# Kernel tuning notes

Hardware: AMD Instinct MI355X
Metric: run time of the kernel (lower is better)

Reference implementation:

```python
import math
import jax, jax.numpy as jnp
import numpy as np

B, V, D, H, DE, DFF = 2, 2048, 1024, 16, 256, 4096
DK = D // H


def setup_inputs() -> dict:
    key = jax.random.key(0)
    ks = jax.random.split(key, 24)
    n = lambda k, shape, s=0.02: (jax.random.normal(k, shape, jnp.float32) * s)
    z = lambda *shape: jnp.zeros(shape, jnp.float32)
    return {
        'x': jax.random.normal(ks[0], (B, V, D), jnp.float32),
        'e_node': jax.random.normal(ks[1], (B, V, DE), jnp.float32),
        'conn': jax.random.uniform(ks[2], (B, V, V), jnp.float32),
        'ln1_g': jnp.ones((D,), jnp.float32), 'ln1_b': z(D),
        'f1w1': n(ks[3], (DE, 2 * D)), 'f1b1': z(2 * D),
        'f1w2': n(ks[4], (2 * D, 2 * D)), 'f1b2': z(2 * D),
        'wq': n(ks[5], (D, D)), 'bq': z(D),
        'wk': n(ks[6], (D, D)), 'bk': z(D),
        'wv': n(ks[7], (D, D)), 'bv': z(D),
        'wp': n(ks[8], (D, D)), 'bp': z(D),
        'ln2_g': jnp.ones((D,), jnp.float32), 'ln2_b': z(D),
        'f2w1': n(ks[9], (DE, 2 * D)), 'f2b1': z(2 * D),
        'f2w2': n(ks[10], (2 * D, 2 * D)), 'f2b2': z(2 * D),
        'ffw1': n(ks[11], (D, DFF)), 'ffb1': z(DFF),
        'ffw2': n(ks[12], (DFF, D)), 'ffb2': z(D),
    }


def _ln(x, g, b):
    m = x.mean(-1, keepdims=True)
    v = ((x - m) ** 2).mean(-1, keepdims=True)
    return (x - m) / jnp.sqrt(v + 1e-5) * g + b


def _film(e, w1, b1, w2, b2):
    h = jax.nn.gelu(e @ w1 + b1, approximate=False)  # torch F.gelu default = exact erf
    gb = h @ w2 + b2
    return jnp.split(gb, 2, axis=-1)  # gamma, beta


def reference(x, e_node, conn, ln1_g, ln1_b, f1w1, f1b1, f1w2, f1b2,
              wq, bq, wk, bk, wv, bv, wp, bp, ln2_g, ln2_b,
              f2w1, f2b1, f2w2, f2b2, ffw1, ffb1, ffw2, ffb2):
    b, v, d = x.shape
    # Pre-norm + FiLM 1
    y = _ln(x, ln1_g, ln1_b)
    g1, be1 = _film(e_node, f1w1, f1b1, f1w2, f1b2)
    y = y * (1.0 + g1) + be1
    # Multi-head attention with additive log(conn) mask
    heads = lambda t: t.reshape(b, v, H, DK).transpose(0, 2, 1, 3)  # [B,h,V,dk]
    Q = heads(y @ wq + bq)
    K = heads(y @ wk + bk)
    Vv = heads(y @ wv + bv)
    logits = jnp.einsum('bhqd,bhkd->bhqk', Q, K) / math.sqrt(DK)
    log_mask = jnp.log(jnp.clip(conn, 0.0, 1.0) + 1e-6)[:, None]  # [B,1,V,V]
    s = logits + log_mask
    s = s - s.max(-1, keepdims=True)
    a = jnp.exp(s)
    a = a / (a.sum(-1, keepdims=True) + 1e-8)
    o = jnp.einsum('bhqk,bhkd->bhqd', a, Vv)
    o = o.transpose(0, 2, 1, 3).reshape(b, v, d)
    x = x + (o @ wp + bp)
    # Pre-norm + FiLM 2 + FFN
    y2 = _ln(x, ln2_g, ln2_b)
    g2, be2 = _film(e_node, f2w1, f2b1, f2w2, f2b2)
    y2 = y2 * (1.0 + g2) + be2
    y2 = jax.nn.gelu(y2 @ ffw1 + ffb1, approximate=False) @ ffw2 + ffb2
    return x + y2
```

## Files before the change

kernel.cpp:

```cpp
#include <hip/hip_runtime.h>
#include <math.h>
#include <stdint.h>

#define B_   2
#define V_   2048
#define D_   1024
#define H_   16
#define DK_  64
#define DE_  256
#define DFF_ 4096
#define M_   (B_*V_)
#define D2_  (2*D_)
#define D3_  (3*D_)

typedef unsigned short u16;
typedef unsigned int   u32;
typedef __bf16 bf16x8 __attribute__((ext_vector_type(8)));
typedef u16    u16x8  __attribute__((ext_vector_type(8)));
typedef u16    u16x4  __attribute__((ext_vector_type(4)));
typedef float  f32x4  __attribute__((ext_vector_type(4)));
typedef u32    u32x2  __attribute__((ext_vector_type(2)));
typedef u32    u32x4  __attribute__((ext_vector_type(4)));

__device__ __forceinline__ float bf2f(u16 u) {
    union { unsigned int i; float f; } z; z.i = ((unsigned int)u) << 16; return z.f;
}
__device__ __forceinline__ u16 f2bf(float f) {
    union { float f; unsigned int i; } z; z.f = f;
    unsigned int x = z.i;
    return (u16)((x + 0x7fffu + ((x >> 16) & 1u)) >> 16);
}
__device__ __forceinline__ float gelu_erf(float v) {
    return 0.5f * v * (1.0f + erff(v * 0.70710678118654752f));
}
__device__ __forceinline__ float ldv(const float* p) { return *p; }
__device__ __forceinline__ float ldv(const u16* p)   { return bf2f(*p); }
__device__ __forceinline__ void  stv(float* p, float v) { *p = v; }
__device__ __forceinline__ void  stv(u16* p,   float v) { *p = f2bf(v); }

__device__ __forceinline__ void gload16(const u16* g, u16* lds)
{
    __builtin_amdgcn_global_load_lds(
        (const __attribute__((address_space(1))) void*)g,
        (__attribute__((address_space(3))) void*)(uintptr_t)lds,
        16, 0, 0);
}

__device__ __forceinline__ void barrier_raw()
{
    asm volatile("" ::: "memory");
    __builtin_amdgcn_s_barrier();
    asm volatile("" ::: "memory");
}

__global__ void convT_k(const float* __restrict__ W, u16* __restrict__ Wt, int K, int N)
{
    __shared__ float tile[32][33];
    const int n0 = blockIdx.x * 32, k0 = blockIdx.y * 32;
    const int tx = threadIdx.x, ty = threadIdx.y;
    #pragma unroll
    for (int j = 0; j < 4; ++j)
        tile[ty * 4 + j][tx] = W[(size_t)(k0 + ty * 4 + j) * N + n0 + tx];
    __syncthreads();
    #pragma unroll
    for (int j = 0; j < 4; ++j)
        Wt[(size_t)(n0 + ty * 4 + j) * K + k0 + tx] = f2bf(tile[tx][ty * 4 + j]);
}

__global__ void conv_k(const float* __restrict__ X, u16* __restrict__ Y)
{
    const int i = (blockIdx.x * 256 + threadIdx.x) * 4;
    f32x4 v = *reinterpret_cast<const f32x4*>(X + i);
    u16x4 o;
    #pragma unroll
    for (int j = 0; j < 4; ++j) o[j] = f2bf(v[j]);
    *reinterpret_cast<u16x4*>(Y + i) = o;
}

__global__ void lmask_k(const float* __restrict__ conn, u16* __restrict__ Lm)
{
    const size_t i = ((size_t)blockIdx.x * 256 + threadIdx.x) * 8;
    f32x4 a = *reinterpret_cast<const f32x4*>(conn + i);
    f32x4 b = *reinterpret_cast<const f32x4*>(conn + i + 4);
    u16x8 o;
    #pragma unroll
    for (int j = 0; j < 4; ++j) {
        o[j]     = f2bf(__log2f(fminf(fmaxf(a[j], 0.f), 1.f) + 1e-6f));
        o[j + 4] = f2bf(__log2f(fminf(fmaxf(b[j], 0.f), 1.f) + 1e-6f));
    }
    *reinterpret_cast<u16x8*>(Lm + i) = o;
}

__global__ void qkvbias_k(const float* __restrict__ bq, const float* __restrict__ bk,
                          const float* __restrict__ bv, float* __restrict__ o)
{
    int i = blockIdx.x * 256 + threadIdx.x;
    o[i] = i < 1024 ? bq[i] : (i < 2048 ? bk[i - 1024] : bv[i - 2048]);
}

template<int EPI, int BN, typename TC, typename TRES>
__launch_bounds__(256)
__global__ void gemm_k(const u16* __restrict__ A, const u16* __restrict__ Wt,
                       const float* __restrict__ bias, const TRES* __restrict__ res,
                       TC* __restrict__ C, int M, int N, int K)
{
    constexpr int NB = BN / 32;
    constexpr int IB = BN / 32;
    __shared__ u16 As[2][128 * 64];
    __shared__ u16 Bs[2][BN * 64];

    const int tid  = threadIdx.x;
    const int lane = tid & 63;
    const int w    = tid >> 6;
    const int wm   = (w >> 1) * 64, wn = (w & 1) * (BN / 2);
    const int m0   = blockIdx.y * 128, n0 = blockIdx.x * BN;
    const int l15  = lane & 15, l4 = lane >> 4;
    const int rStage = lane >> 3;

    int rrA[4], ccA[4];
    #pragma unroll
    for (int i = 0; i < 4; ++i) {
        rrA[i] = w * 32 + i * 8 + rStage;
        ccA[i] = (lane & 7) ^ (rrA[i] & 7);
    }
    int rrB[IB], ccB[IB];
    #pragma unroll
    for (int i = 0; i < IB; ++i) {
        rrB[i] = w * (BN / 4) + i * 8 + rStage;
        ccB[i] = (lane & 7) ^ (rrB[i] & 7);
    }

    auto stage = [&](int kt, int dd) {
        const int k0 = kt * 64;
        #pragma unroll
        for (int i = 0; i < 4; ++i)
            gload16(A + (size_t)(m0 + rrA[i]) * K + k0 + ccA[i] * 8, &As[dd][w * 2048 + i * 512]);
        #pragma unroll
        for (int i = 0; i < IB; ++i)
            gload16(Wt + (size_t)(n0 + rrB[i]) * K + k0 + ccB[i] * 8, &Bs[dd][w * (BN * 16) + i * 512]);
    };

    f32x4 acc[4][NB] = {};
    const int NT = K / 64;

    stage(0, 0);

    for (int t = 0; t < NT; ++t) {
        const int d = t & 1;
        barrier_raw();
        if (t + 1 < NT) {
            stage(t + 1, d ^ 1);
            if constexpr (BN == 128) asm volatile("s_waitcnt vmcnt(8)" ::: "memory");
            else                     asm volatile("s_waitcnt vmcnt(6)" ::: "memory");
        } else {
            asm volatile("s_waitcnt vmcnt(0)" ::: "memory");
        }
        barrier_raw();
        __builtin_amdgcn_sched_barrier(0);

        #pragma unroll
        for (int kk = 0; kk < 2; ++kk) {
            bf16x8 a[4], b[NB];
            #pragma unroll
            for (int mb = 0; mb < 4; ++mb) {
                int r  = wm + mb * 16 + l15;
                int ph = (kk * 4 + l4) ^ (r & 7);
                a[mb] = *reinterpret_cast<const bf16x8*>(&As[d][r * 64 + ph * 8]);
            }
            #pragma unroll
            for (int nb = 0; nb < NB; ++nb) {
                int r  = wn + nb * 16 + l15;
                int ph = (kk * 4 + l4) ^ (r & 7);
                b[nb] = *reinterpret_cast<const bf16x8*>(&Bs[d][r * 64 + ph * 8]);
            }
            #pragma unroll
            for (int mb = 0; mb < 4; ++mb)
                #pragma unroll
                for (int nb = 0; nb < NB; ++nb)
                    acc[mb][nb] = __builtin_amdgcn_mfma_f32_16x16x32_bf16(a[mb], b[nb], acc[mb][nb], 0, 0, 0);
        }
    }

    #pragma unroll
    for (int nb = 0; nb < NB; ++nb) {
        int col = n0 + wn + nb * 16 + l15;
        float bv = bias[col];
        #pragma unroll
        for (int mb = 0; mb < 4; ++mb) {
            #pragma unroll
            for (int i = 0; i < 4; ++i) {
                int row = m0 + wm + mb * 16 + l4 * 4 + i;
                float v = acc[mb][nb][i] + bv;
                if (EPI == 1) v = gelu_erf(v);
                if (EPI == 2) v += ldv(res + (size_t)row * N + col);
                stv(C + (size_t)row * N + col, v);
            }
        }
    }
}

template<typename TX>
__launch_bounds__(256)
__global__ void lnfilm_k(const TX* __restrict__ X, const u16* __restrict__ GB,
                         const float* __restrict__ g, const float* __restrict__ bb,
                         u16* __restrict__ Y)
{
    const int row = blockIdx.x;
    const int tid = threadIdx.x;
    const int d0  = tid * 4;
    const TX* xr = X + (size_t)row * D_ + d0;
    float xs[4], s = 0.f, sq = 0.f;
    if constexpr (sizeof(TX) == 4) {
        f32x4 v4 = *reinterpret_cast<const f32x4*>(xr);
        #pragma unroll
        for (int j = 0; j < 4; ++j) { xs[j] = v4[j]; s += xs[j]; sq += xs[j] * xs[j]; }
    } else {
        u16x4 v4 = *reinterpret_cast<const u16x4*>(xr);
        #pragma unroll
        for (int j = 0; j < 4; ++j) { xs[j] = bf2f(v4[j]); s += xs[j]; sq += xs[j] * xs[j]; }
    }
    #pragma unroll
    for (int off = 32; off; off >>= 1) {
        s  += __shfl_xor(s, off);
        sq += __shfl_xor(sq, off);
    }
    __shared__ float rs[4], rq[4];
    const int w = tid >> 6;
    if ((tid & 63) == 0) { rs[w] = s; rq[w] = sq; }
    __syncthreads();
    s  = rs[0] + rs[1] + rs[2] + rs[3];
    sq = rq[0] + rq[1] + rq[2] + rq[3];
    const float mean = s * (1.0f / D_);
    const float var  = sq * (1.0f / D_) - mean * mean;
    const float rstd = rsqrtf(fmaxf(var, 0.f) + 1e-5f);
    const u16* gbr = GB + (size_t)row * D2_ + d0;
    u16x4 g4 = *reinterpret_cast<const u16x4*>(gbr);
    u16x4 b4 = *reinterpret_cast<const u16x4*>(gbr + D_);
    f32x4 gg = *reinterpret_cast<const f32x4*>(g + d0);
    f32x4 bv = *reinterpret_cast<const f32x4*>(bb + d0);
    u16x4 o;
    #pragma unroll
    for (int j = 0; j < 4; ++j) {
        float v = (xs[j] - mean) * rstd * gg[j] + bv[j];
        v = v * (1.0f + bf2f(g4[j])) + bf2f(b4[j]);
        o[j] = f2bf(v);
    }
    *reinterpret_cast<u16x4*>(Y + (size_t)row * D_ + d0) = o;
}

__launch_bounds__(256)
__global__ void attn_k(const u16* __restrict__ Q, const u16* __restrict__ K,
                       const u16* __restrict__ Vv, const u16* __restrict__ Lm,
                       u16* __restrict__ O, int ld)
{
    __shared__ u16 Ks[64 * 64];
    __shared__ u16 Vs[64 * 64];
    __shared__ u16 Lms[128 * 64];
    __shared__ u16 Ps[128 * 72];

    const int blk = blockIdx.x;
    const int qt  = blk & 15;
    const int h   = (blk >> 4) & 15;
    const int b   = blk >> 8;
    const int q0  = qt * 128;
    const int tid = threadIdx.x, lane = tid & 63, w = tid >> 6;
    const int l15 = lane & 15, l4 = lane >> 4;
    const size_t bV = (size_t)b * V_;

    bf16x8 qa[2][2];
    #pragma unroll
    for (int g = 0; g < 2; ++g) {
        const u16* qp = Q + (bV + q0 + w * 32 + g * 16 + l15) * ld + h * 64;
        u16x8 r0 = *reinterpret_cast<const u16x8*>(qp + l4 * 8);
        u16x8 r1 = *reinterpret_cast<const u16x8*>(qp + 32 + l4 * 8);
        u16x8 s0, s1;
        #pragma unroll
        for (int j = 0; j < 8; ++j) {
            s0[j] = f2bf(bf2f(r0[j]) * 0.125f);
            s1[j] = f2bf(bf2f(r1[j]) * 0.125f);
        }
        union { u16x8 u; bf16x8 h; } c0, c1;
        c0.u = s0; c1.u = s1;
        qa[g][0] = c0.h; qa[g][1] = c1.h;
    }

    const int rStage = (lane >> 3);
    const int cSw    = ((lane & 7) ^ rStage) * 8;
    const int vK     = ((lane >> 5) << 2) + ((lane & 7) >> 1);
    const int vDk    = ((lane >> 3) & 3) * 16 + (lane & 1) * 8;
    const u32 vaddr  = (u32)(uintptr_t)&Vs[0] + (l4 << 10) + (l15 << 3);

    int lmOff[4];
    #pragma unroll
    for (int kb = 0; kb < 4; ++kb)
        lmOff[kb] = ((((kb << 1) | (l4 >> 1)) ^ (l15 & 7)) << 3);

    const float LOG2E = 1.44269504088896f;
    float lrp[2] = {0.f, 0.f};
    f32x4 o4[2][4] = {};

    for (int kt = 0; kt < V_ / 64; ++kt) {
        const int k0 = kt * 64;
        if (kt) __syncthreads();
        #pragma unroll
        for (int i = 0; i < 2; ++i) {
            int r  = i * 32 + w * 8 + rStage;
            int kv = i * 32 + w * 8 + vK;
            gload16(K  + (bV + k0 + r)  * ld + h * 64 + cSw, &Ks[i * 2048 + w * 512]);
            gload16(Vv + (bV + k0 + kv) * ld + h * 64 + vDk, &Vs[i * 2048 + w * 512]);
        }
        #pragma unroll
        for (int i = 0; i < 4; ++i) {
            int r = i * 32 + w * 8 + rStage;
            gload16(Lm + (bV + q0 + r) * (size_t)V_ + k0 + cSw, &Lms[i * 2048 + w * 512]);
        }
        __syncthreads();

        #pragma unroll
        for (int g = 0; g < 2; ++g) {
            f32x4 s[4];
            #pragma unroll
            for (int kb = 0; kb < 4; ++kb) {
                int row = (kb * 16 + l15) * 64;
                bf16x8 k0f = *reinterpret_cast<const bf16x8*>(&Ks[row + ((l4 ^ (l15 & 7)) * 8)]);
                bf16x8 k1f = *reinterpret_cast<const bf16x8*>(&Ks[row + (((l4 + 4) ^ (l15 & 7)) * 8)]);
                f32x4 z = {};
                z = __builtin_amdgcn_mfma_f32_16x16x32_bf16(k0f, qa[g][0], z, 0, 0, 0);
                z = __builtin_amdgcn_mfma_f32_16x16x32_bf16(k1f, qa[g][1], z, 0, 0, 0);
                s[kb] = z;
            }
            const int lmRow = w * 32 + g * 16 + l15;
            const u16* lmBase = &Lms[lmRow * 64 + (l4 & 1) * 4];
            u16* psW = &Ps[lmRow * 72 + l4 * 4];
            #pragma unroll
            for (int kb = 0; kb < 4; ++kb) {
                u16x4 lm4 = *reinterpret_cast<const u16x4*>(lmBase + lmOff[kb]);
                float p0, p1, p2, p3;
                float t0 = fmaf(s[kb][0], LOG2E, bf2f(lm4[0]));
                float t1 = fmaf(s[kb][1], LOG2E, bf2f(lm4[1]));
                float t2 = fmaf(s[kb][2], LOG2E, bf2f(lm4[2]));
                float t3 = fmaf(s[kb][3], LOG2E, bf2f(lm4[3]));
                asm("v_exp_f32 %0, %1" : "=v"(p0) : "v"(t0));
                asm("v_exp_f32 %0, %1" : "=v"(p1) : "v"(t1));
                asm("v_exp_f32 %0, %1" : "=v"(p2) : "v"(t2));
                asm("v_exp_f32 %0, %1" : "=v"(p3) : "v"(t3));
                lrp[g] += (p0 + p1) + (p2 + p3);
                u32 d0, d1;
                asm("v_cvt_pk_bf16_f32 %0, %1, %2" : "=v"(d0) : "v"(p0), "v"(p1));
                asm("v_cvt_pk_bf16_f32 %0, %1, %2" : "=v"(d1) : "v"(p2), "v"(p3));
                u32x2 dd = {d0, d1};
                *reinterpret_cast<u32x2*>(psW + kb * 16) = dd;
            }
        }

        union VU { u32x4 u; bf16x8 h; };
        VU vb[2][4];
        #pragma unroll
        for (int c2 = 0; c2 < 2; ++c2) {
            u32 a0 = vaddr + c2 * 4096;
            u32x2 t0, t1, t2, t3, t4, t5, t6, t7;
            asm volatile("ds_read_b64_tr_b16 %0, %1"            : "=v"(t0) : "v"(a0));
            asm volatile("ds_read_b64_tr_b16 %0, %1 offset:512" : "=v"(t1) : "v"(a0));
            asm volatile("ds_read_b64_tr_b16 %0, %1 offset:128" : "=v"(t2) : "v"(a0));
            asm volatile("ds_read_b64_tr_b16 %0, %1 offset:640" : "=v"(t3) : "v"(a0));
            asm volatile("ds_read_b64_tr_b16 %0, %1 offset:256" : "=v"(t4) : "v"(a0));
            asm volatile("ds_read_b64_tr_b16 %0, %1 offset:768" : "=v"(t5) : "v"(a0));
            asm volatile("ds_read_b64_tr_b16 %0, %1 offset:384" : "=v"(t6) : "v"(a0));
            asm volatile("ds_read_b64_tr_b16 %0, %1 offset:896" : "=v"(t7) : "v"(a0));
            asm volatile("s_waitcnt lgkmcnt(0)" ::: "memory");
            __builtin_amdgcn_sched_barrier(0);
            vb[c2][0].u = (u32x4){t0.x, t0.y, t1.x, t1.y};
            vb[c2][1].u = (u32x4){t2.x, t2.y, t3.x, t3.y};
            vb[c2][2].u = (u32x4){t4.x, t4.y, t5.x, t5.y};
            vb[c2][3].u = (u32x4){t6.x, t6.y, t7.x, t7.y};
        }
        #pragma unroll
        for (int g = 0; g < 2; ++g) {
            const u16* pr = &Ps[(w * 32 + g * 16 + l15) * 72];
            bf16x8 pa0 = *reinterpret_cast<const bf16x8*>(pr + l4 * 8);
            bf16x8 pa1 = *reinterpret_cast<const bf16x8*>(pr + 32 + l4 * 8);
            #pragma unroll
            for (int nb = 0; nb < 4; ++nb) {
                o4[g][nb] = __builtin_amdgcn_mfma_f32_16x16x32_bf16(pa0, vb[0][nb].h, o4[g][nb], 0, 0, 0);
                o4[g][nb] = __builtin_amdgcn_mfma_f32_16x16x32_bf16(pa1, vb[1][nb].h, o4[g][nb], 0, 0, 0);
            }
        }
    }

    #pragma unroll
    for (int g = 0; g < 2; ++g) {
        float v = lrp[g];
        v += __shfl_xor(v, 16);
        v += __shfl_xor(v, 32);
        #pragma unroll
        for (int i = 0; i < 4; ++i) {
            float lw = __shfl(v, (lane & 48) | ((l4 << 2) + i));
            float rcp = 1.0f / (lw + 1e-8f);
            int q = q0 + w * 32 + g * 16 + l4 * 4 + i;
            u16* op = O + (bV + q) * D_ + h * 64;
            #pragma unroll
            for (int nb = 0; nb < 4; ++nb)
                op[nb * 16 + l15] = f2bf(o4[g][nb][i] * rcp);
        }
    }
}

extern "C" void kernel_launch(void* const* d_in, const int* in_sizes, int n_in,
                              void* d_out, int out_size, void* d_ws, size_t ws_size,
                              hipStream_t stream)
{
    (void)in_sizes; (void)n_in; (void)out_size; (void)ws_size;
    const float* x    = (const float*)d_in[0];
    const float* e    = (const float*)d_in[1];
    const float* conn = (const float*)d_in[2];
    const float* ln1g = (const float*)d_in[3];
    const float* ln1b = (const float*)d_in[4];
    const float* f1w1 = (const float*)d_in[5];
    const float* f1b1 = (const float*)d_in[6];
    const float* f1w2 = (const float*)d_in[7];
    const float* f1b2 = (const float*)d_in[8];
    const float* wq   = (const float*)d_in[9];
    const float* bq   = (const float*)d_in[10];
    const float* wk   = (const float*)d_in[11];
    const float* bk   = (const float*)d_in[12];
    const float* wv   = (const float*)d_in[13];
    const float* bv   = (const float*)d_in[14];
    const float* wp   = (const float*)d_in[15];
    const float* bp   = (const float*)d_in[16];
    const float* ln2g = (const float*)d_in[17];
    const float* ln2b = (const float*)d_in[18];
    const float* f2w1 = (const float*)d_in[19];
    const float* f2b1 = (const float*)d_in[20];
    const float* f2w2 = (const float*)d_in[21];
    const float* f2b2 = (const float*)d_in[22];
    const float* ffw1 = (const float*)d_in[23];
    const float* ffb1 = (const float*)d_in[24];
    const float* ffw2 = (const float*)d_in[25];
    const float* ffb2 = (const float*)d_in[26];
    float* out = (float*)d_out;

    char* ws = (char*)d_ws;
    const size_t MB = 1u << 20;
    u16*   Lm    = (u16*)(ws + 0);
    u16*   e_bf  = (u16*)(ws + 16 * MB);
    u16*   h     = (u16*)(ws + 18 * MB);
    u16*   wt2   = (u16*)(ws + 34 * MB);
    u16*   wt8   = (u16*)(ws + 36 * MB);
    u16*   gb    = (u16*)(ws + 44 * MB);
    u16*   y     = (u16*)(ws + 60 * MB);
    u16*   wqkvt = (u16*)(ws + 18 * MB);
    u16*   qkv   = (u16*)(ws + 24 * MB);
    float* qkvb  = (float*)(ws + 71 * MB);
    u16*   o     = (u16*)(ws + 48 * MB);
    u16*   xnew  = (u16*)(ws + 64 * MB);
    u16*   h2    = (u16*)(ws + 18 * MB);
    u16*   gb2   = (u16*)(ws + 44 * MB);
    u16*   y2    = (u16*)(ws + 0);
    u16*   ffw1t = (u16*)(ws + 8 * MB);
    u16*   t     = (u16*)(ws + 16 * MB);
    u16*   ffw2t = (u16*)(ws + 48 * MB);

    dim3 blk(256), tblk(32, 8);
    #define CONVT(W, WT, K, N) convT_k<<<dim3((N)/32, (K)/32), tblk, 0, stream>>>(W, WT, K, N)

    conv_k <<<(M_*DE_)/1024, blk, 0, stream>>>(e, e_bf);
    lmask_k<<<(B_*(size_t)V_*V_)/2048, blk, 0, stream>>>(conn, Lm);

    CONVT(f1w1, wt2, DE_, D2_);
    gemm_k<1, 64, u16, u16><<<dim3(D2_/64, M_/128), blk, 0, stream>>>(e_bf, wt2, f1b1, (const u16*)nullptr, h, M_, D2_, DE_);
    CONVT(f1w2, wt8, D2_, D2_);
    gemm_k<0, 64, u16, u16><<<dim3(D2_/64, M_/128), blk, 0, stream>>>(h, wt8, f1b2, (const u16*)nullptr, gb, M_, D2_, D2_);
    lnfilm_k<float><<<M_, blk, 0, stream>>>(x, gb, ln1g, ln1b, y);
    CONVT(wq, wqkvt,                 D_, D_);
    CONVT(wk, wqkvt + 1024 * 1024,   D_, D_);
    CONVT(wv, wqkvt + 2048 * 1024,   D_, D_);
    qkvbias_k<<<D3_/256, blk, 0, stream>>>(bq, bk, bv, qkvb);
    gemm_k<0, 128, u16, u16><<<dim3(D3_/128, M_/128), blk, 0, stream>>>(y, wqkvt, qkvb, (const u16*)nullptr, qkv, M_, D3_, D_);
    attn_k<<<B_*H_*(V_/128), blk, 0, stream>>>(qkv, qkv + 1024, qkv + 2048, Lm, o, D3_);
    CONVT(wp, wt2, D_, D_);
    gemm_k<2, 64, u16, float><<<dim3(D_/64, M_/128), blk, 0, stream>>>(o, wt2, bp, x, xnew, M_, D_, D_);
    CONVT(f2w1, wt2, DE_, D2_);
    gemm_k<1, 64, u16, u16><<<dim3(D2_/64, M_/128), blk, 0, stream>>>(e_bf, wt2, f2b1, (const u16*)nullptr, h2, M_, D2_, DE_);
    CONVT(f2w2, wt8, D2_, D2_);
    gemm_k<0, 64, u16, u16><<<dim3(D2_/64, M_/128), blk, 0, stream>>>(h2, wt8, f2b2, (const u16*)nullptr, gb2, M_, D2_, D2_);
    lnfilm_k<u16><<<M_, blk, 0, stream>>>(xnew, gb2, ln2g, ln2b, y2);
    CONVT(ffw1, ffw1t, D_, DFF_);
    gemm_k<1, 128, u16, u16><<<dim3(DFF_/128, M_/128), blk, 0, stream>>>(y2, ffw1t, ffb1, (const u16*)nullptr, t, M_, DFF_, D_);
    CONVT(ffw2, ffw2t, DFF_, D_);
    gemm_k<2, 64, float, u16><<<dim3(D_/64, M_/128), blk, 0, stream>>>(t, ffw2t, ffb2, xnew, out, M_, D_, DFF_);
    #undef CONVT
}
```

Baseline: 402.3 us.

## Split attention over key halves with combine kernel; stage GEMM epilogue through LDS

The attention kernel now splits the key range into two halves, doubling the block count. Each half writes unnormalized partial outputs and row sums, and a new combine kernel adds them and normalizes. This targets low occupancy from only 256 attention blocks, at the cost of extra global traffic and one more launch. The combine only adds partials without max rescaling, so it relies on both halves using the same max. The GEMM epilogue now stages results in swizzled LDS as bf16 and writes vectorized, coalesced stores with the residual added afterward. That adds a bf16 rounding step before the residual add.

Result: slower. 414.7 us (+3.1%).

```diff
diff --git a/kernel.cpp b/kernel.cpp
--- a/kernel.cpp
+++ b/kernel.cpp
@@ -33,10 +33,6 @@
 __device__ __forceinline__ float gelu_erf(float v) {
     return 0.5f * v * (1.0f + erff(v * 0.70710678118654752f));
 }
-__device__ __forceinline__ float ldv(const float* p) { return *p; }
-__device__ __forceinline__ float ldv(const u16* p)   { return bf2f(*p); }
-__device__ __forceinline__ void  stv(float* p, float v) { *p = v; }
-__device__ __forceinline__ void  stv(u16* p,   float v) { *p = f2bf(v); }
 
 __device__ __forceinline__ void gload16(const u16* g, u16* lds)
 {
@@ -96,6 +92,22 @@
 {
     int i = blockIdx.x * 256 + threadIdx.x;
     o[i] = i < 1024 ? bq[i] : (i < 2048 ? bk[i - 1024] : bv[i - 2048]);
+}
+
+__global__ void combine_k(const u16* __restrict__ Op, const float* __restrict__ Lp,
+                          u16* __restrict__ O)
+{
+    const size_t c = ((size_t)blockIdx.x * 256 + threadIdx.x) * 8;
+    const int row = (int)(c >> 10);
+    const int hh  = (int)((c & 1023) >> 6);
+    u16x8 a  = *reinterpret_cast<const u16x8*>(Op + c);
+    u16x8 b2 = *reinterpret_cast<const u16x8*>(Op + (size_t)M_ * D_ + c);
+    float l = Lp[(size_t)row * H_ + hh] + Lp[((size_t)M_ + row) * H_ + hh];
+    float rcp = 1.0f / (l + 1e-8f);
+    u16x8 o;
+    #pragma unroll
+    for (int j = 0; j < 8; ++j) o[j] = f2bf((bf2f(a[j]) + bf2f(b2[j])) * rcp);
+    *reinterpret_cast<u16x8*>(O + c) = o;
 }
 
 template<int EPI, int BN, typename TC, typename TRES>
@@ -181,20 +193,69 @@
         }
     }
 
+    barrier_raw();
+    u16* Cs = (u16*)&As[0][0];
     #pragma unroll
     for (int nb = 0; nb < NB; ++nb) {
-        int col = n0 + wn + nb * 16 + l15;
-        float bv = bias[col];
+        int col  = wn + nb * 16 + l15;
+        int colx = col ^ (l4 << 4);
+        float bv = bias[n0 + col];
         #pragma unroll
         for (int mb = 0; mb < 4; ++mb) {
             #pragma unroll
             for (int i = 0; i < 4; ++i) {
-                int row = m0 + wm + mb * 16 + l4 * 4 + i;
                 float v = acc[mb][nb][i] + bv;
                 if (EPI == 1) v = gelu_erf(v);
-                if (EPI == 2) v += ldv(res + (size_t)row * N + col);
-                stv(C + (size_t)row * N + col, v);
-            }
+                Cs[(wm + mb * 16 + l4 * 4 + i) * BN + colx] = f2bf(v);
+            }
+        }
+    }
+    asm volatile("s_waitcnt lgkmcnt(0)" ::: "memory");
+    barrier_raw();
+    constexpr int CPR = BN / 8;
+    #pragma unroll
+    for (int p = 0; p < (128 * CPR) / 256; ++p) {
+        int c   = p * 256 + tid;
+        int row = c / CPR;
+        int cl  = (c % CPR) * 8;
+        int cp  = cl ^ (((row >> 2) & 3) << 4);
+        u16x8 vv = *reinterpret_cast<const u16x8*>(&Cs[row * BN + cp]);
+        size_t gidx = (size_t)(m0 + row) * N + n0 + cl;
+        if constexpr (sizeof(TC) == 2) {
+            if (EPI == 2) {
+                if constexpr (sizeof(TRES) == 2) {
+                    u16x8 rr = *reinterpret_cast<const u16x8*>((const u16*)res + gidx);
+                    #pragma unroll
+                    for (int j = 0; j < 8; ++j) vv[j] = f2bf(bf2f(vv[j]) + bf2f(rr[j]));
+                } else {
+                    f32x4 r0 = *reinterpret_cast<const f32x4*>((const float*)res + gidx);
+                    f32x4 r1 = *reinterpret_cast<const f32x4*>((const float*)res + gidx + 4);
+                    #pragma unroll
+                    for (int j = 0; j < 4; ++j) {
+                        vv[j]     = f2bf(bf2f(vv[j])     + r0[j]);
+                        vv[j + 4] = f2bf(bf2f(vv[j + 4]) + r1[j]);
+                    }
+                }
+            }
+            *reinterpret_cast<u16x8*>((u16*)C + gidx) = vv;
+        } else {
+            f32x4 o0, o1;
+            #pragma unroll
+            for (int j = 0; j < 4; ++j) { o0[j] = bf2f(vv[j]); o1[j] = bf2f(vv[j + 4]); }
+            if (EPI == 2) {
+                if constexpr (sizeof(TRES) == 2) {
+                    u16x8 rr = *reinterpret_cast<const u16x8*>((const u16*)res + gidx);
+                    #pragma unroll
+                    for (int j = 0; j < 4; ++j) { o0[j] += bf2f(rr[j]); o1[j] += bf2f(rr[j + 4]); }
+                } else {
+                    f32x4 r0 = *reinterpret_cast<const f32x4*>((const float*)res + gidx);
+                    f32x4 r1 = *reinterpret_cast<const f32x4*>((const float*)res + gidx + 4);
+                    #pragma unroll
+                    for (int j = 0; j < 4; ++j) { o0[j] += r0[j]; o1[j] += r1[j]; }
+                }
+            }
+            *reinterpret_cast<f32x4*>((float*)C + gidx)     = o0;
+            *reinterpret_cast<f32x4*>((float*)C + gidx + 4) = o1;
         }
     }
 }
@@ -251,18 +312,19 @@
 __launch_bounds__(256)
 __global__ void attn_k(const u16* __restrict__ Q, const u16* __restrict__ K,
                        const u16* __restrict__ Vv, const u16* __restrict__ Lm,
-                       u16* __restrict__ O, int ld)
+                       u16* __restrict__ Op, float* __restrict__ Lp, int ld)
 {
     __shared__ u16 Ks[64 * 64];
     __shared__ u16 Vs[64 * 64];
     __shared__ u16 Lms[128 * 64];
     __shared__ u16 Ps[128 * 72];
 
-    const int blk = blockIdx.x;
-    const int qt  = blk & 15;
-    const int h   = (blk >> 4) & 15;
-    const int b   = blk >> 8;
-    const int q0  = qt * 128;
+    const int blk  = blockIdx.x;
+    const int half = blk >> 9;
+    const int qt   = blk & 15;
+    const int h    = (blk >> 4) & 15;
+    const int b    = (blk >> 8) & 1;
+    const int q0   = qt * 128;
     const int tid = threadIdx.x, lane = tid & 63, w = tid >> 6;
     const int l15 = lane & 15, l4 = lane >> 4;
     const size_t bV = (size_t)b * V_;
@@ -299,9 +361,10 @@
     float lrp[2] = {0.f, 0.f};
     f32x4 o4[2][4] = {};
 
-    for (int kt = 0; kt < V_ / 64; ++kt) {
+    const int kt0 = half * 16, kt1 = kt0 + 16;
+    for (int kt = kt0; kt < kt1; ++kt) {
         const int k0 = kt * 64;
-        if (kt) __syncthreads();
+        if (kt > kt0) __syncthreads();
         #pragma unroll
         for (int i = 0; i < 2; ++i) {
             int r  = i * 32 + w * 8 + rStage;
@@ -387,20 +450,21 @@
         }
     }
 
+    u16* Ob = Op + (size_t)half * M_ * D_;
     #pragma unroll
     for (int g = 0; g < 2; ++g) {
         float v = lrp[g];
         v += __shfl_xor(v, 16);
         v += __shfl_xor(v, 32);
+        if ((lane >> 4) == 0)
+            Lp[((size_t)half * M_ + bV + q0 + w * 32 + g * 16 + l15) * H_ + h] = v;
         #pragma unroll
         for (int i = 0; i < 4; ++i) {
-            float lw = __shfl(v, (lane & 48) | ((l4 << 2) + i));
-            float rcp = 1.0f / (lw + 1e-8f);
             int q = q0 + w * 32 + g * 16 + l4 * 4 + i;
-            u16* op = O + (bV + q) * D_ + h * 64;
+            u16* op = Ob + (bV + q) * D_ + h * 64;
             #pragma unroll
             for (int nb = 0; nb < 4; ++nb)
-                op[nb * 16 + l15] = f2bf(o4[g][nb][i] * rcp);
+                op[nb * 16 + l15] = f2bf(o4[g][nb][i]);
         }
     }
 }
@@ -452,6 +516,7 @@
     u16*   qkv   = (u16*)(ws + 24 * MB);
     float* qkvb  = (float*)(ws + 71 * MB);
     u16*   o     = (u16*)(ws + 48 * MB);
+    float* Lp    = (float*)(ws + 64 * MB);
     u16*   xnew  = (u16*)(ws + 64 * MB);
     u16*   h2    = (u16*)(ws + 18 * MB);
     u16*   gb2   = (u16*)(ws + 44 * MB);
@@ -476,7 +541,8 @@
     CONVT(wv, wqkvt + 2048 * 1024,   D_, D_);
     qkvbias_k<<<D3_/256, blk, 0, stream>>>(bq, bk, bv, qkvb);
     gemm_k<0, 128, u16, u16><<<dim3(D3_/128, M_/128), blk, 0, stream>>>(y, wqkvt, qkvb, (const u16*)nullptr, qkv, M_, D3_, D_);
-    attn_k<<<B_*H_*(V_/128), blk, 0, stream>>>(qkv, qkv + 1024, qkv + 2048, Lm, o, D3_);
+    attn_k<<<2*B_*H_*(V_/128), blk, 0, stream>>>(qkv, qkv + 1024, qkv + 2048, Lm, o, Lp, D3_);
+    combine_k<<<(M_*(size_t)D_)/2048, blk, 0, stream>>>(o, Lp, o);
     CONVT(wp, wt2, D_, D_);
     gemm_k<2, 64, u16, float><<<dim3(D_/64, M_/128), blk, 0, stream>>>(o, wt2, bp, x, xnew, M_, D_, D_);
     CONVT(f2w1, wt2, DE_, D2_);
```

## Fuse FiLM second GEMM with LayerNorm modulation and batch QKV weight transposes

Applied to the files above, without the earlier changes.

The second FiLM GEMM now computes the gamma and beta column tiles together in one block and applies LayerNorm plus FiLM modulation in its epilogue. Row mean and rstd come from a new small stats kernel. This removes the bf16 gamma/beta intermediate round trip and the separate lnfilm launch. The three Q/K/V weight transposes are merged into one 3D-grid launch. The epilogue reads X and stats with scattered per-element loads, and the gamma/beta values stay in fp32 instead of being rounded to bf16.

After: 382.4 us. 1.05x faster.

```diff
diff --git a/kernel.cpp b/kernel.cpp
--- a/kernel.cpp
+++ b/kernel.cpp
@@ -67,6 +67,23 @@
         Wt[(size_t)(n0 + ty * 4 + j) * K + k0 + tx] = f2bf(tile[tx][ty * 4 + j]);
 }
 
+__global__ void convT3_k(const float* __restrict__ W0, const float* __restrict__ W1,
+                         const float* __restrict__ W2, u16* __restrict__ Wt)
+{
+    __shared__ float tile[32][33];
+    const float* W = blockIdx.z == 0 ? W0 : (blockIdx.z == 1 ? W1 : W2);
+    u16* dst = Wt + (size_t)blockIdx.z * D_ * D_;
+    const int n0 = blockIdx.x * 32, k0 = blockIdx.y * 32;
+    const int tx = threadIdx.x, ty = threadIdx.y;
+    #pragma unroll
+    for (int j = 0; j < 4; ++j)
+        tile[ty * 4 + j][tx] = W[(size_t)(k0 + ty * 4 + j) * D_ + n0 + tx];
+    __syncthreads();
+    #pragma unroll
+    for (int j = 0; j < 4; ++j)
+        dst[(size_t)(n0 + ty * 4 + j) * D_ + k0 + tx] = f2bf(tile[tx][ty * 4 + j]);
+}
+
 __global__ void conv_k(const float* __restrict__ X, u16* __restrict__ Y)
 {
     const int i = (blockIdx.x * 256 + threadIdx.x) * 4;
@@ -96,6 +113,42 @@
 {
     int i = blockIdx.x * 256 + threadIdx.x;
     o[i] = i < 1024 ? bq[i] : (i < 2048 ? bk[i - 1024] : bv[i - 2048]);
+}
+
+template<typename TX>
+__launch_bounds__(256)
+__global__ void xstats_k(const TX* __restrict__ X, float* __restrict__ stats)
+{
+    const int row = blockIdx.x;
+    const int tid = threadIdx.x;
+    const TX* xr = X + (size_t)row * D_ + tid * 4;
+    float s = 0.f, sq = 0.f;
+    if constexpr (sizeof(TX) == 4) {
+        f32x4 v4 = *reinterpret_cast<const f32x4*>(xr);
+        #pragma unroll
+        for (int j = 0; j < 4; ++j) { s += v4[j]; sq += v4[j] * v4[j]; }
+    } else {
+        u16x4 v4 = *reinterpret_cast<const u16x4*>(xr);
+        #pragma unroll
+        for (int j = 0; j < 4; ++j) { float v = bf2f(v4[j]); s += v; sq += v * v; }
+    }
+    #pragma unroll
+    for (int off = 32; off; off >>= 1) {
+        s  += __shfl_xor(s, off);
+        sq += __shfl_xor(sq, off);
+    }
+    __shared__ float rs[4], rq[4];
+    const int w = tid >> 6;
+    if ((tid & 63) == 0) { rs[w] = s; rq[w] = sq; }
+    __syncthreads();
+    if (tid == 0) {
+        s  = rs[0] + rs[1] + rs[2] + rs[3];
+        sq = rq[0] + rq[1] + rq[2] + rq[3];
+        float mean = s * (1.0f / D_);
+        float var  = sq * (1.0f / D_) - mean * mean;
+        stats[row * 2]     = mean;
+        stats[row * 2 + 1] = rsqrtf(fmaxf(var, 0.f) + 1e-5f);
+    }
 }
 
 template<int EPI, int BN, typename TC, typename TRES>
@@ -201,51 +254,112 @@
 
 template<typename TX>
 __launch_bounds__(256)
-__global__ void lnfilm_k(const TX* __restrict__ X, const u16* __restrict__ GB,
-                         const float* __restrict__ g, const float* __restrict__ bb,
-                         u16* __restrict__ Y)
-{
-    const int row = blockIdx.x;
-    const int tid = threadIdx.x;
-    const int d0  = tid * 4;
-    const TX* xr = X + (size_t)row * D_ + d0;
-    float xs[4], s = 0.f, sq = 0.f;
-    if constexpr (sizeof(TX) == 4) {
-        f32x4 v4 = *reinterpret_cast<const f32x4*>(xr);
-        #pragma unroll
-        for (int j = 0; j < 4; ++j) { xs[j] = v4[j]; s += xs[j]; sq += xs[j] * xs[j]; }
-    } else {
-        u16x4 v4 = *reinterpret_cast<const u16x4*>(xr);
-        #pragma unroll
-        for (int j = 0; j < 4; ++j) { xs[j] = bf2f(v4[j]); s += xs[j]; sq += xs[j] * xs[j]; }
-    }
-    #pragma unroll
-    for (int off = 32; off; off >>= 1) {
-        s  += __shfl_xor(s, off);
-        sq += __shfl_xor(sq, off);
-    }
-    __shared__ float rs[4], rq[4];
-    const int w = tid >> 6;
-    if ((tid & 63) == 0) { rs[w] = s; rq[w] = sq; }
-    __syncthreads();
-    s  = rs[0] + rs[1] + rs[2] + rs[3];
-    sq = rq[0] + rq[1] + rq[2] + rq[3];
-    const float mean = s * (1.0f / D_);
-    const float var  = sq * (1.0f / D_) - mean * mean;
-    const float rstd = rsqrtf(fmaxf(var, 0.f) + 1e-5f);
-    const u16* gbr = GB + (size_t)row * D2_ + d0;
-    u16x4 g4 = *reinterpret_cast<const u16x4*>(gbr);
-    u16x4 b4 = *reinterpret_cast<const u16x4*>(gbr + D_);
-    f32x4 gg = *reinterpret_cast<const f32x4*>(g + d0);
-    f32x4 bv = *reinterpret_cast<const f32x4*>(bb + d0);
-    u16x4 o;
-    #pragma unroll
-    for (int j = 0; j < 4; ++j) {
-        float v = (xs[j] - mean) * rstd * gg[j] + bv[j];
-        v = v * (1.0f + bf2f(g4[j])) + bf2f(b4[j]);
-        o[j] = f2bf(v);
-    }
-    *reinterpret_cast<u16x4*>(Y + (size_t)row * D_ + d0) = o;
+__global__ void gemmfilm_k(const u16* __restrict__ A, const u16* __restrict__ Wt,
+                           const float* __restrict__ b2, const TX* __restrict__ X,
+                           const float* __restrict__ stats,
+                           const float* __restrict__ lng, const float* __restrict__ lnb,
+                           u16* __restrict__ Y)
+{
+    constexpr int Kc = D2_;
+    __shared__ u16 As[2][128 * 64];
+    __shared__ u16 Bs[2][128 * 64];
+
+    const int tid  = threadIdx.x;
+    const int lane = tid & 63;
+    const int w    = tid >> 6;
+    const int wm   = (w >> 1) * 64, wn = (w & 1) * 32;
+    const int m0   = blockIdx.y * 128, n0 = blockIdx.x * 64;
+    const int l15  = lane & 15, l4 = lane >> 4;
+    const int rStage = lane >> 3;
+
+    int rrA[4], ccA[4];
+    #pragma unroll
+    for (int i = 0; i < 4; ++i) {
+        rrA[i] = w * 32 + i * 8 + rStage;
+        ccA[i] = (lane & 7) ^ (rrA[i] & 7);
+    }
+    int rowB[4], ccB[4], grB[4];
+    #pragma unroll
+    for (int i = 0; i < 4; ++i) {
+        int lr = w * 16 + (i & 1) * 8 + rStage;
+        rowB[i] = (i < 2 ? 0 : 64) + lr;
+        grB[i]  = (i < 2 ? n0 : D_ + n0) + lr;
+        ccB[i]  = (lane & 7) ^ (lr & 7);
+    }
+
+    auto stage = [&](int kt, int dd) {
+        const int k0 = kt * 64;
+        #pragma unroll
+        for (int i = 0; i < 4; ++i)
+            gload16(A + (size_t)(m0 + rrA[i]) * Kc + k0 + ccA[i] * 8, &As[dd][w * 2048 + i * 512]);
+        #pragma unroll
+        for (int i = 0; i < 4; ++i)
+            gload16(Wt + (size_t)grB[i] * Kc + k0 + ccB[i] * 8,
+                    &Bs[dd][((i < 2 ? 0 : 64) + w * 16 + (i & 1) * 8) * 64]);
+    };
+
+    f32x4 accG[4][2] = {}, accB2[4][2] = {};
+    const int NT = Kc / 64;
+
+    stage(0, 0);
+
+    for (int t = 0; t < NT; ++t) {
+        const int d = t & 1;
+        barrier_raw();
+        if (t + 1 < NT) {
+            stage(t + 1, d ^ 1);
+            asm volatile("s_waitcnt vmcnt(8)" ::: "memory");
+        } else {
+            asm volatile("s_waitcnt vmcnt(0)" ::: "memory");
+        }
+        barrier_raw();
+        __builtin_amdgcn_sched_barrier(0);
+
+        #pragma unroll
+        for (int kk = 0; kk < 2; ++kk) {
+            bf16x8 a[4], bg[2], bb[2];
+            #pragma unroll
+            for (int mb = 0; mb < 4; ++mb) {
+                int r  = wm + mb * 16 + l15;
+                int ph = (kk * 4 + l4) ^ (r & 7);
+                a[mb] = *reinterpret_cast<const bf16x8*>(&As[d][r * 64 + ph * 8]);
+            }
+            #pragma unroll
+            for (int nb = 0; nb < 2; ++nb) {
+                int r  = wn + nb * 16 + l15;
+                int ph = (kk * 4 + l4) ^ (r & 7);
+                bg[nb] = *reinterpret_cast<const bf16x8*>(&Bs[d][r * 64 + ph * 8]);
+                bb[nb] = *reinterpret_cast<const bf16x8*>(&Bs[d][(64 + r) * 64 + ph * 8]);
+            }
+            #pragma unroll
+            for (int mb = 0; mb < 4; ++mb)
+                #pragma unroll
+                for (int nb = 0; nb < 2; ++nb) {
+                    accG[mb][nb]  = __builtin_amdgcn_mfma_f32_16x16x32_bf16(a[mb], bg[nb], accG[mb][nb], 0, 0, 0);
+                    accB2[mb][nb] = __builtin_amdgcn_mfma_f32_16x16x32_bf16(a[mb], bb[nb], accB2[mb][nb], 0, 0, 0);
+                }
+        }
+    }
+
+    #pragma unroll
+    for (int nb = 0; nb < 2; ++nb) {
+        int col = n0 + wn + nb * 16 + l15;
+        float gb_ = b2[col], bb_ = b2[D_ + col];
+        float lg = lng[col], lb = lnb[col];
+        #pragma unroll
+        for (int mb = 0; mb < 4; ++mb) {
+            #pragma unroll
+            for (int i = 0; i < 4; ++i) {
+                int row = m0 + wm + mb * 16 + l4 * 4 + i;
+                float mean = stats[row * 2], rstd = stats[row * 2 + 1];
+                float xv = ldv(X + (size_t)row * D_ + col);
+                float gamma = accG[mb][nb][i] + gb_;
+                float beta  = accB2[mb][nb][i] + bb_;
+                float v = ((xv - mean) * rstd * lg + lb) * (1.0f + gamma) + beta;
+                Y[(size_t)row * D_ + col] = f2bf(v);
+            }
+        }
+    }
 }
 
 __launch_bounds__(256)
@@ -445,8 +559,8 @@
     u16*   e_bf  = (u16*)(ws + 16 * MB);
     u16*   h     = (u16*)(ws + 18 * MB);
     u16*   wt2   = (u16*)(ws + 34 * MB);
+    float* stats = (float*)(ws + 35 * MB);
     u16*   wt8   = (u16*)(ws + 36 * MB);
-    u16*   gb    = (u16*)(ws + 44 * MB);
     u16*   y     = (u16*)(ws + 60 * MB);
     u16*   wqkvt = (u16*)(ws + 18 * MB);
     u16*   qkv   = (u16*)(ws + 24 * MB);
@@ -454,7 +568,6 @@
     u16*   o     = (u16*)(ws + 48 * MB);
     u16*   xnew  = (u16*)(ws + 64 * MB);
     u16*   h2    = (u16*)(ws + 18 * MB);
-    u16*   gb2   = (u16*)(ws + 44 * MB);
     u16*   y2    = (u16*)(ws + 0);
     u16*   ffw1t = (u16*)(ws + 8 * MB);
     u16*   t     = (u16*)(ws + 16 * MB);
@@ -468,12 +581,10 @@
 
     CONVT(f1w1, wt2, DE_, D2_);
     gemm_k<1, 64, u16, u16><<<dim3(D2_/64, M_/128), blk, 0, stream>>>(e_bf, wt2, f1b1, (const u16*)nullptr, h, M_, D2_, DE_);
+    xstats_k<float><<<M_, blk, 0, stream>>>(x, stats);
     CONVT(f1w2, wt8, D2_, D2_);
-    gemm_k<0, 64, u16, u16><<<dim3(D2_/64, M_/128), blk, 0, stream>>>(h, wt8, f1b2, (const u16*)nullptr, gb, M_, D2_, D2_);
-    lnfilm_k<float><<<M_, blk, 0, stream>>>(x, gb, ln1g, ln1b, y);
-    CONVT(wq, wqkvt,                 D_, D_);
-    CONVT(wk, wqkvt + 1024 * 1024,   D_, D_);
-    CONVT(wv, wqkvt + 2048 * 1024,   D_, D_);
+    gemmfilm_k<float><<<dim3(D_/64, M_/128), blk, 0, stream>>>(h, wt8, f1b2, x, stats, ln1g, ln1b, y);
+    convT3_k<<<dim3(D_/32, D_/32, 3), tblk, 0, stream>>>(wq, wk, wv, wqkvt);
     qkvbias_k<<<D3_/256, blk, 0, stream>>>(bq, bk, bv, qkvb);
     gemm_k<0, 128, u16, u16><<<dim3(D3_/128, M_/128), blk, 0, stream>>>(y, wqkvt, qkvb, (const u16*)nullptr, qkv, M_, D3_, D_);
     attn_k<<<B_*H_*(V_/128), blk, 0, stream>>>(qkv, qkv + 1024, qkv + 2048, Lm, o, D3_);
@@ -481,9 +592,9 @@
     gemm_k<2, 64, u16, float><<<dim3(D_/64, M_/128), blk, 0, stream>>>(o, wt2, bp, x, xnew, M_, D_, D_);
     CONVT(f2w1, wt2, DE_, D2_);
     gemm_k<1, 64, u16, u16><<<dim3(D2_/64, M_/128), blk, 0, stream>>>(e_bf, wt2, f2b1, (const u16*)nullptr, h2, M_, D2_, DE_);
+    xstats_k<u16><<<M_, blk, 0, stream>>>(xnew, stats);
     CONVT(f2w2, wt8, D2_, D2_);
-    gemm_k<0, 64, u16, u16><<<dim3(D2_/64, M_/128), blk, 0, stream>>>(h2, wt8, f2b2, (const u16*)nullptr, gb2, M_, D2_, D2_);
-    lnfilm_k<u16><<<M_, blk, 0, stream>>>(xnew, gb2, ln2g, ln2b, y2);
+    gemmfilm_k<u16><<<dim3(D_/64, M_/128), blk, 0, stream>>>(h2, wt8, f2b2, xnew, stats, ln2g, ln2b, y2);
     CONVT(ffw1, ffw1t, D_, DFF_);
     gemm_k<1, 128, u16, u16><<<dim3(DFF_/128, M_/128), blk, 0, stream>>>(y2, ffw1t, ffb1, (const u16*)nullptr, t, M_, DFF_, D_);
     CONVT(ffw2, ffw2t, DFF_, D_);
```
